# Kernel optimization log

Hardware: AMD Instinct MI355X
Metric: run time of the kernel (lower is better)

The kernel has to match this reference:

```python
import jax, jax.numpy as jnp
import numpy as np

N = 262144          # pixels (512x512 image)
F = 2               # in_features (x, y)
K = 13              # num_frequencies
H = 256             # dim_hidden
OUT = 3             # out_features (RGB)
TILES = [1, 4, 16, 64, 256]   # prod(tile_dims[i]) per layer
PE_DIM = F + 2 * F * K        # 54


def setup_inputs() -> dict:
    key = jax.random.key(0)
    ks = jax.random.split(key, 2 * len(TILES) + 3)
    inp = {"coords": jax.random.uniform(ks[0], (N, F), dtype=jnp.float32)}
    d_in = PE_DIM
    for i, t in enumerate(TILES):
        # kaiming-uniform-like scale; biases init to zero as in the module
        bound = float(np.sqrt(6.0 / d_in))
        inp[f"w{i}"] = jax.random.uniform(ks[1 + i], (t, d_in, H), dtype=jnp.float32,
                                           minval=-bound, maxval=bound)
        inp[f"b{i}"] = jnp.zeros((H,), dtype=jnp.float32)
        d_in = H
    bound = float(np.sqrt(6.0 / H))
    inp["w_last"] = jax.random.uniform(ks[-1], (OUT, H), dtype=jnp.float32,
                                        minval=-bound, maxval=bound)
    inp["b_last"] = jnp.zeros((OUT,), dtype=jnp.float32)
    return inp


def _pos_enc(coords):
    # NeRF positional encoding, concat order: coords, then for each freq i,
    # for each feature j: sin(2^i * pi * c_j), cos(2^i * pi * c_j)
    freqs = (2.0 ** jnp.arange(K, dtype=jnp.float32)) * np.pi      # [K]
    ang = coords[:, None, :] * freqs[None, :, None]                # [N, K, F]
    enc = jnp.stack([jnp.sin(ang), jnp.cos(ang)], axis=-1)         # [N, K, F, 2]
    enc = enc.reshape(coords.shape[0], 2 * K * F)
    return jnp.concatenate([coords, enc], axis=-1)                 # [N, PE_DIM]


def reference(coords, w0, b0, w1, b1, w2, b2, w3, b3, w4, b4, w_last, b_last):
    x = _pos_enc(coords)                                           # [N, 54]
    for w, b in ((w0, b0), (w1, b1), (w2, b2), (w3, b3), (w4, b4)):
        t = w.shape[0]
        x = x.reshape(t, -1, x.shape[-1])                          # [T, N/T, d_in]
        x = jnp.einsum('tnd,tdo->tno', x, w) + b                   # per-tile GEMM
        x = jnp.where(x > 0, x, 0.2 * x)                           # LeakyReLU(0.2)
    x = x.reshape(-1, H)                                           # [N, H]
    return x @ w_last.T + b_last                                   # [N, OUT]
```

## Files before the change

### kernel.cpp

```cpp
#include <hip/hip_runtime.h>
#include <stdint.h>

typedef uint32_t u32;
typedef short s16x8 __attribute__((ext_vector_type(8)));
typedef float f32x16 __attribute__((ext_vector_type(16)));
typedef u32 u32x2 __attribute__((ext_vector_type(2)));
typedef u32 u32x4 __attribute__((ext_vector_type(4)));

#define NPIX   262144
#define HD     256
#define NTHR   512

#define ACT_BYTES  131072
#define WBUF_BYTES 16384
#define LDS_BYTES  (ACT_BYTES + 2 * WBUF_BYTES)

#define B0_OFF  0u
#define B1_OFF  32768u
#define B2_OFF  557056u
#define B3_OFF  2654208u
#define B4_OFF  11042816u
#define BH_OFF  44597248u
#define BLOB_TOTAL 44613632u
#define F_W1 2048u
#define F_W2 34816u
#define F_W3 165888u
#define F_W4 690176u
#define F_WH 2787328u
#define F_END 2788352u

typedef __attribute__((address_space(3))) u32 as3_u32;
typedef __attribute__((address_space(1))) u32 as1_u32;

__device__ __forceinline__ void gload16(const void* g, void* l) {
    __builtin_amdgcn_global_load_lds((const as1_u32*)(uintptr_t)g,
                                     (as3_u32*)(u32)(uintptr_t)l, 16, 0, 0);
}

__device__ __forceinline__ u32 bfpair(float a, float b) {
    u32 ua = __builtin_bit_cast(u32, a);
    u32 ub = __builtin_bit_cast(u32, b);
    ua = (ua + 0x7FFFu + ((ua >> 16) & 1u)) >> 16;
    ub = (ub + 0x7FFFu + ((ub >> 16) & 1u)) >> 16;
    return ua | (ub << 16);
}
__device__ __forceinline__ u32 act_off(int row, int colByte) {
    return (u32)((row << 9) + (colByte ^ ((row & 7) << 4)));
}
__device__ __forceinline__ u32 w_off32(int col, int kByte) {
    return (u32)((col << 6) + (kByte ^ (((col >> 1) & 3) << 4)));
}

extern "C" __global__ __launch_bounds__(256)
void loe_prepass(const float* __restrict__ w0, const float* __restrict__ w1,
                 const float* __restrict__ w2, const float* __restrict__ w3,
                 const float* __restrict__ w4, const float* __restrict__ wl,
                 char* __restrict__ ws)
{
    const u32 f = blockIdx.x * 256 + threadIdx.x;
    if (f >= F_END) return;
    float v[8];
    char* dst;
    if (f < F_W1) {
        const u32 s = f >> 10, r2 = f & 1023, col = r2 >> 2, kg = r2 & 3;
        const u32 k0 = s * 32 + kg * 8;
        #pragma unroll
        for (int j = 0; j < 8; ++j)
            v[j] = (k0 + j < 54) ? w0[(k0 + j) * HD + col] : 0.0f;
        dst = ws + B0_OFF + s * 16384 + w_off32(col, kg * 16);
    } else if (f < F_WH) {
        const float* W; size_t boff; u32 fl;
        if (f < F_W2)      { W = w1; boff = B1_OFF; fl = f - F_W1; }
        else if (f < F_W3) { W = w2; boff = B2_OFF; fl = f - F_W2; }
        else if (f < F_W4) { W = w3; boff = B3_OFF; fl = f - F_W3; }
        else               { W = w4; boff = B4_OFF; fl = f - F_W4; }
        const u32 t = fl >> 13, r = fl & 8191, s = r >> 10, r2 = r & 1023;
        const u32 col = r2 >> 2, kg = r2 & 3;
        const u32 k0 = s * 32 + kg * 8;
        const float* src = W + (size_t)t * 65536 + (size_t)k0 * HD + col;
        #pragma unroll
        for (int j = 0; j < 8; ++j) v[j] = src[(size_t)j * HD];
        dst = ws + boff + (size_t)t * 131072 + s * 16384 + w_off32(col, kg * 16);
    } else {
        const u32 fl = f - F_WH;
        const u32 col = fl >> 5, kg = fl & 31, k0 = kg * 8;
        #pragma unroll
        for (int j = 0; j < 8; ++j)
            v[j] = (col < 3) ? wl[col * HD + k0 + j] : 0.0f;
        dst = ws + BH_OFF + col * 512 + ((kg * 16) ^ ((col & 7) << 4));
    }
    u32x4 pk;
    pk.x = bfpair(v[0], v[1]); pk.y = bfpair(v[2], v[3]);
    pk.z = bfpair(v[4], v[5]); pk.w = bfpair(v[6], v[7]);
    *reinterpret_cast<u32x4*>(dst) = pk;
}

extern "C" __global__ __launch_bounds__(NTHR, 2)
void loe_fused_pre(const float* __restrict__ coords,
                   const float* __restrict__ b0, const float* __restrict__ b1,
                   const float* __restrict__ b2, const float* __restrict__ b3,
                   const float* __restrict__ b4, const float* __restrict__ bl,
                   const char* __restrict__ blob,
                   float* __restrict__ out)
{
    extern __shared__ char lds[];
    char* wbufg = lds + ACT_BYTES;

    const int tid  = threadIdx.x;
    const int lane = tid & 63;
    const int wv   = tid >> 6;
    const int wr   = wv >> 2;
    const int wc   = wv & 3;
    const int l31  = lane & 31;
    const int lhi  = lane >> 5;

    const int bid  = (int)blockIdx.x;
    const int pb   = ((bid & 7) << 7) | (bid >> 3);
    const int pix0 = pb << 8;

    int g = 0;

    auto stage = [&](const char* src, int parity) {
        const char* s0 = src + wv * 2048 + (size_t)lane * 16;
        char* d0 = wbufg + parity * WBUF_BYTES + wv * 2048;
        gload16(s0, d0);
        gload16(s0 + 1024, d0 + 1024);
    };

    const char* b0p = blob + B0_OFF;
    const char* b1p = blob + B1_OFF + (size_t)(pb >> 8) * 131072;
    const char* b2p = blob + B2_OFF + (size_t)(pb >> 6) * 131072;
    const char* b3p = blob + B3_OFF + (size_t)(pb >> 4) * 131072;
    const char* b4p = blob + B4_OFF + (size_t)(pb >> 2) * 131072;
    const char* bHp = blob + BH_OFF;

    stage(b0p, 0);

    {
        const int p = tid >> 1;
        const int h = tid & 1;
        const float2 c2 = reinterpret_cast<const float2*>(coords)[pix0 + p];
        const float cf[2] = {c2.x, c2.y};
        #pragma unroll
        for (int u = 0; u < 32; u += 2) {
            float v[2];
            #pragma unroll
            for (int q = 0; q < 2; ++q) {
                const int c = h * 32 + u + q;
                float val;
                if (c < 2) val = cf[c];
                else if (c - 2 >= 52) val = 0.0f;
                else {
                    const int e = c - 2;
                    const float a = cf[(e >> 1) & 1] * (float)(1 << (e >> 2));
                    val = (e & 1) ? cospif(a) : sinpif(a);
                }
                v[q] = val;
            }
            *reinterpret_cast<u32*>(lds + act_off(p, (h * 32 + u) * 2)) = bfpair(v[0], v[1]);
        }
    }

    f32x16 acc[4][2];

    auto init_acc = [&](const float* Bias) {
        #pragma unroll
        for (int ct = 0; ct < 2; ++ct)
            #pragma unroll
            for (int q = 0; q < 4; ++q) {
                const float4 bv = *reinterpret_cast<const float4*>(Bias + wc * 64 + ct * 32 + q * 8 + lhi * 4);
                #pragma unroll
                for (int pt = 0; pt < 4; ++pt) {
                    acc[pt][ct][q * 4 + 0] = bv.x; acc[pt][ct][q * 4 + 1] = bv.y;
                    acc[pt][ct][q * 4 + 2] = bv.z; acc[pt][ct][q * 4 + 3] = bv.w;
                }
            }
    };

    auto epilogue = [&]() {
        #pragma unroll
        for (int ct = 0; ct < 2; ++ct)
            #pragma unroll
            for (int q = 0; q < 4; ++q) {
                const int oc0 = wc * 64 + ct * 32 + q * 8 + lhi * 4;
                #pragma unroll
                for (int pt = 0; pt < 4; ++pt) {
                    const int p = wr * 128 + pt * 32 + l31;
                    float x[4];
                    #pragma unroll
                    for (int j = 0; j < 4; ++j) {
                        const float v = acc[pt][ct][q * 4 + j];
                        x[j] = fmaxf(v, 0.2f * v);
                    }
                    u32x2 w2v;
                    w2v.x = bfpair(x[0], x[1]);
                    w2v.y = bfpair(x[2], x[3]);
                    *reinterpret_cast<u32x2*>(lds + act_off(p, oc0 * 2)) = w2v;
                }
            }
    };

    auto run_layer = [&](int S, const char* cur, const char* nxt, const float* Bias) {
        init_acc(Bias);
        for (int s = 0; s < S; ++s) {
            __syncthreads();
            const char* pf = (s + 1 < S) ? cur + (size_t)(s + 1) * 16384 : nxt;
            stage(pf, (g + 1) & 1);
            const char* wbw = wbufg + (g & 1) * WBUF_BYTES;
            const int kbase = s * 64;
            #pragma unroll
            for (int kt = 0; kt < 2; ++kt) {
                const int kb = kt * 32 + lhi * 16;
                s16x8 wf[2], af[4];
                #pragma unroll
                for (int ct = 0; ct < 2; ++ct)
                    wf[ct] = *reinterpret_cast<const s16x8*>(wbw + w_off32(wc * 64 + ct * 32 + l31, kb));
                #pragma unroll
                for (int pt = 0; pt < 4; ++pt)
                    af[pt] = *reinterpret_cast<const s16x8*>(lds + act_off(wr * 128 + pt * 32 + l31, kbase + kb));
                #pragma unroll
                for (int pt = 0; pt < 4; ++pt)
                    #pragma unroll
                    for (int ct = 0; ct < 2; ++ct)
                        acc[pt][ct] = __builtin_amdgcn_mfma_f32_32x32x16_bf16(wf[ct], af[pt], acc[pt][ct], 0, 0, 0);
            }
            ++g;
        }
        __syncthreads();
        epilogue();
    };

    run_layer(2, b0p, b1p, b0);
    run_layer(8, b1p, b2p, b1);
    run_layer(8, b2p, b3p, b2);
    run_layer(8, b3p, b4p, b3);
    run_layer(8, b4p, bHp, b4);

    __syncthreads();
    {
        const char* hw = wbufg + (g & 1) * WBUF_BYTES;
        f32x16 a;
        #pragma unroll
        for (int r = 0; r < 16; ++r) a[r] = 0.0f;
        #pragma unroll
        for (int kt = 0; kt < 16; ++kt) {
            const int kb = kt * 32 + lhi * 16;
            s16x8 wf = *reinterpret_cast<const s16x8*>(hw + l31 * 512 + (kb ^ ((l31 & 7) << 4)));
            s16x8 af = *reinterpret_cast<const s16x8*>(lds + act_off(wv * 32 + l31, kb));
            a = __builtin_amdgcn_mfma_f32_32x32x16_bf16(wf, af, a, 0, 0, 0);
        }
        if (lhi == 0) {
            const int p = pix0 + wv * 32 + l31;
            out[p * 3 + 0] = a[0] + bl[0];
            out[p * 3 + 1] = a[1] + bl[1];
            out[p * 3 + 2] = a[2] + bl[2];
        }
    }
}

extern "C" __global__ __launch_bounds__(NTHR, 2)
void loe_fused_fb(const float* __restrict__ coords,
                  const float* __restrict__ w0, const float* __restrict__ b0,
                  const float* __restrict__ w1, const float* __restrict__ b1,
                  const float* __restrict__ w2, const float* __restrict__ b2,
                  const float* __restrict__ w3, const float* __restrict__ b3,
                  const float* __restrict__ w4, const float* __restrict__ b4,
                  const float* __restrict__ wl, const float* __restrict__ bl,
                  float* __restrict__ out)
{
    extern __shared__ char lds[];
    const int tid  = threadIdx.x;
    const int lane = tid & 63;
    const int wv   = tid >> 6;
    const int wr   = wv >> 2;
    const int wc   = wv & 3;
    const int l31  = lane & 31;
    const int lhi  = lane >> 5;
    const int bid  = (int)blockIdx.x;
    const int pb   = ((bid & 7) << 7) | (bid >> 3);
    const int pix0 = pb << 8;
    const int scol = tid & 255;
    const int kh   = tid >> 8;

    float st[16];
    auto load_plain = [&](const float* W, int s) {
        const float* src = W + (size_t)(s * 32 + kh * 16) * HD + scol;
        #pragma unroll
        for (int j = 0; j < 16; ++j) st[j] = src[(size_t)j * HD];
    };
    auto load_guard = [&](const float* W, int s) {
        #pragma unroll
        for (int j = 0; j < 16; ++j) {
            const int k = s * 32 + kh * 16 + j;
            st[j] = (k < 54) ? W[k * HD + scol] : 0.0f;
        }
    };
    load_guard(w0, 0);
    {
        const int p = tid >> 1;
        const int h = tid & 1;
        const float2 c2 = reinterpret_cast<const float2*>(coords)[pix0 + p];
        const float cf[2] = {c2.x, c2.y};
        #pragma unroll
        for (int u = 0; u < 32; u += 2) {
            float v[2];
            #pragma unroll
            for (int q = 0; q < 2; ++q) {
                const int c = h * 32 + u + q;
                float val;
                if (c < 2) val = cf[c];
                else if (c - 2 >= 52) val = 0.0f;
                else {
                    const int e = c - 2;
                    const float a = cf[(e >> 1) & 1] * (float)(1 << (e >> 2));
                    val = (e & 1) ? cospif(a) : sinpif(a);
                }
                v[q] = val;
            }
            *reinterpret_cast<u32*>(lds + act_off(p, (h * 32 + u) * 2)) = bfpair(v[0], v[1]);
        }
    }
    f32x16 acc[4][2];
    int g = 0;
    auto epilogue = [&](const float* Bias) {
        #pragma unroll
        for (int ct = 0; ct < 2; ++ct)
            #pragma unroll
            for (int q = 0; q < 4; ++q) {
                const int oc0 = wc * 64 + ct * 32 + q * 8 + lhi * 4;
                const float4 bv = *reinterpret_cast<const float4*>(Bias + oc0);
                const float bj[4] = {bv.x, bv.y, bv.z, bv.w};
                #pragma unroll
                for (int pt = 0; pt < 4; ++pt) {
                    const int p = wr * 128 + pt * 32 + l31;
                    float x[4];
                    #pragma unroll
                    for (int j = 0; j < 4; ++j) {
                        float v = acc[pt][ct][q * 4 + j] + bj[j];
                        x[j] = (v > 0.0f) ? v : 0.2f * v;
                    }
                    u32x2 wv2;
                    wv2.x = bfpair(x[0], x[1]);
                    wv2.y = bfpair(x[2], x[3]);
                    *reinterpret_cast<u32x2*>(lds + act_off(p, oc0 * 2)) = wv2;
                }
            }
    };
    auto run_layer = [&](int S, const float* Wcur, const float* Wnext,
                         const float* Bias, bool guard) {
        #pragma unroll
        for (int pt = 0; pt < 4; ++pt)
            #pragma unroll
            for (int ct = 0; ct < 2; ++ct)
                #pragma unroll
                for (int r = 0; r < 16; ++r) acc[pt][ct][r] = 0.0f;
        for (int s = 0; s < S; ++s) {
            char* wbw = lds + ACT_BYTES + ((g & 1) ? WBUF_BYTES : 0);
            u32x4 pk0, pk1;
            pk0.x = bfpair(st[0], st[1]);   pk0.y = bfpair(st[2], st[3]);
            pk0.z = bfpair(st[4], st[5]);   pk0.w = bfpair(st[6], st[7]);
            pk1.x = bfpair(st[8], st[9]);   pk1.y = bfpair(st[10], st[11]);
            pk1.z = bfpair(st[12], st[13]); pk1.w = bfpair(st[14], st[15]);
            *reinterpret_cast<u32x4*>(wbw + w_off32(scol, kh * 32))      = pk0;
            *reinterpret_cast<u32x4*>(wbw + w_off32(scol, kh * 32 + 16)) = pk1;
            if (s + 1 < S) { if (guard) load_guard(Wcur, s + 1); else load_plain(Wcur, s + 1); }
            else if (Wnext) load_plain(Wnext, 0);
            __syncthreads();
            const int kbase = s * 64;
            #pragma unroll
            for (int kt = 0; kt < 2; ++kt) {
                const int kb = kt * 32 + lhi * 16;
                s16x8 wf[2], af[4];
                #pragma unroll
                for (int ct = 0; ct < 2; ++ct)
                    wf[ct] = *reinterpret_cast<const s16x8*>(wbw + w_off32(wc * 64 + ct * 32 + l31, kb));
                #pragma unroll
                for (int pt = 0; pt < 4; ++pt)
                    af[pt] = *reinterpret_cast<const s16x8*>(lds + act_off(wr * 128 + pt * 32 + l31, kbase + kb));
                #pragma unroll
                for (int pt = 0; pt < 4; ++pt)
                    #pragma unroll
                    for (int ct = 0; ct < 2; ++ct)
                        acc[pt][ct] = __builtin_amdgcn_mfma_f32_32x32x16_bf16(wf[ct], af[pt], acc[pt][ct], 0, 0, 0);
            }
            ++g;
        }
        __syncthreads();
        epilogue(Bias);
    };
    const float* w1t = w1 + (size_t)(pb >> 8) * 65536;
    const float* w2t = w2 + (size_t)(pb >> 6) * 65536;
    const float* w3t = w3 + (size_t)(pb >> 4) * 65536;
    const float* w4t = w4 + (size_t)(pb >> 2) * 65536;
    run_layer(2, w0,  w1t, b0, true);
    run_layer(8, w1t, w2t, b1, false);
    run_layer(8, w2t, w3t, b2, false);
    run_layer(8, w3t, w4t, b3, false);
    run_layer(8, w4t, nullptr, b4, false);
    char* hw = lds + ACT_BYTES;
    #pragma unroll
    for (int rep = 0; rep < 2; ++rep) {
        const int task = rep * NTHR + tid;
        const int col  = task & 31;
        const int kg   = task >> 5;
        float v[8];
        #pragma unroll
        for (int j = 0; j < 8; ++j)
            v[j] = (col < 3) ? wl[col * HD + kg * 8 + j] : 0.0f;
        u32x4 pk;
        pk.x = bfpair(v[0], v[1]); pk.y = bfpair(v[2], v[3]);
        pk.z = bfpair(v[4], v[5]); pk.w = bfpair(v[6], v[7]);
        *reinterpret_cast<u32x4*>(hw + col * 512 + ((kg * 16) ^ ((col & 7) << 4))) = pk;
    }
    __syncthreads();
    {
        f32x16 a;
        #pragma unroll
        for (int r = 0; r < 16; ++r) a[r] = 0.0f;
        #pragma unroll
        for (int kt = 0; kt < 16; ++kt) {
            const int kb = kt * 32 + lhi * 16;
            s16x8 wf = *reinterpret_cast<const s16x8*>(hw + l31 * 512 + (kb ^ ((l31 & 7) << 4)));
            s16x8 af = *reinterpret_cast<const s16x8*>(lds + act_off(wv * 32 + l31, kb));
            a = __builtin_amdgcn_mfma_f32_32x32x16_bf16(wf, af, a, 0, 0, 0);
        }
        if (lhi == 0) {
            const int p = pix0 + wv * 32 + l31;
            out[p * 3 + 0] = a[0] + bl[0];
            out[p * 3 + 1] = a[1] + bl[1];
            out[p * 3 + 2] = a[2] + bl[2];
        }
    }
}

extern "C" void kernel_launch(void* const* d_in, const int* in_sizes, int n_in,
                              void* d_out, int out_size, void* d_ws, size_t ws_size,
                              hipStream_t stream) {
    (void)in_sizes; (void)n_in; (void)out_size;
    const float* coords = (const float*)d_in[0];
    const float* w0 = (const float*)d_in[1];  const float* b0 = (const float*)d_in[2];
    const float* w1 = (const float*)d_in[3];  const float* b1 = (const float*)d_in[4];
    const float* w2 = (const float*)d_in[5];  const float* b2 = (const float*)d_in[6];
    const float* w3 = (const float*)d_in[7];  const float* b3 = (const float*)d_in[8];
    const float* w4 = (const float*)d_in[9];  const float* b4 = (const float*)d_in[10];
    const float* wl = (const float*)d_in[11]; const float* bl = (const float*)d_in[12];
    float* out = (float*)d_out;

    if (ws_size >= (size_t)BLOB_TOTAL) {
        (void)hipFuncSetAttribute((const void*)loe_fused_pre,
                                  hipFuncAttributeMaxDynamicSharedMemorySize, LDS_BYTES);
        loe_prepass<<<dim3(F_END / 256), dim3(256), 0, stream>>>(
            w0, w1, w2, w3, w4, wl, (char*)d_ws);
        loe_fused_pre<<<dim3(NPIX / 256), dim3(NTHR), LDS_BYTES, stream>>>(
            coords, b0, b1, b2, b3, b4, bl, (const char*)d_ws, out);
    } else {
        (void)hipFuncSetAttribute((const void*)loe_fused_fb,
                                  hipFuncAttributeMaxDynamicSharedMemorySize, LDS_BYTES);
        loe_fused_fb<<<dim3(NPIX / 256), dim3(NTHR), LDS_BYTES, stream>>>(
            coords, w0, b0, w1, b1, w2, b2, w3, b3, w4, b4, wl, bl, out);
    }
}
```

Measured before the change: 188.4 us.

## Load weight MFMA fragments directly from global into registers, drop LDS weight staging

The main kernel now uses 128-pixel blocks of 256 threads, and each wave owns a 64-column slice of every layer. Weight fragments are prepacked in MFMA lane order so they can be read straight from global/L2 into registers, with a one-step software prefetch. This removes the LDS weight double buffer and most per-step barriers and halves LDS to 64KB, which should allow more resident blocks. In exchange each block re-reads full weight tiles from L2 with no LDS sharing across waves, and it processes fewer pixels per block.

```diff
diff --git a/kernel.cpp b/kernel.cpp
--- a/kernel.cpp
+++ b/kernel.cpp
@@ -9,11 +9,11 @@
 
 #define NPIX   262144
 #define HD     256
-#define NTHR   512
-
-#define ACT_BYTES  131072
-#define WBUF_BYTES 16384
-#define LDS_BYTES  (ACT_BYTES + 2 * WBUF_BYTES)
+
+#define FTHR      256
+#define PXB       128
+#define NBLK      (NPIX / PXB)
+#define ACT_LDS   65536
 
 #define B0_OFF  0u
 #define B1_OFF  32768u
@@ -29,13 +29,9 @@
 #define F_WH 2787328u
 #define F_END 2788352u
 
-typedef __attribute__((address_space(3))) u32 as3_u32;
-typedef __attribute__((address_space(1))) u32 as1_u32;
-
-__device__ __forceinline__ void gload16(const void* g, void* l) {
-    __builtin_amdgcn_global_load_lds((const as1_u32*)(uintptr_t)g,
-                                     (as3_u32*)(u32)(uintptr_t)l, 16, 0, 0);
-}
+#define ACT_BYTES  131072
+#define WBUF_BYTES 16384
+#define FB_LDS     (ACT_BYTES + 2 * WBUF_BYTES)
 
 __device__ __forceinline__ u32 bfpair(float a, float b) {
     u32 ua = __builtin_bit_cast(u32, a);
@@ -45,7 +41,7 @@
     return ua | (ub << 16);
 }
 __device__ __forceinline__ u32 act_off(int row, int colByte) {
-    return (u32)((row << 9) + (colByte ^ ((row & 7) << 4)));
+    return (u32)((row << 9) + (colByte ^ ((row & 31) << 4)));
 }
 __device__ __forceinline__ u32 w_off32(int col, int kByte) {
     return (u32)((col << 6) + (kByte ^ (((col >> 1) & 3) << 4)));
@@ -62,32 +58,36 @@
     float v[8];
     char* dst;
     if (f < F_W1) {
-        const u32 s = f >> 10, r2 = f & 1023, col = r2 >> 2, kg = r2 & 3;
-        const u32 k0 = s * 32 + kg * 8;
+        const u32 kk = f >> 9, fb = (f >> 6) & 7, lane = f & 63;
+        const u32 l31 = lane & 31, lhi = lane >> 5;
+        const u32 k0 = kk * 16 + lhi * 8, col = fb * 32 + l31;
         #pragma unroll
         for (int j = 0; j < 8; ++j)
             v[j] = (k0 + j < 54) ? w0[(k0 + j) * HD + col] : 0.0f;
-        dst = ws + B0_OFF + s * 16384 + w_off32(col, kg * 16);
+        dst = ws + B0_OFF + (size_t)f * 16;
     } else if (f < F_WH) {
         const float* W; size_t boff; u32 fl;
         if (f < F_W2)      { W = w1; boff = B1_OFF; fl = f - F_W1; }
         else if (f < F_W3) { W = w2; boff = B2_OFF; fl = f - F_W2; }
         else if (f < F_W4) { W = w3; boff = B3_OFF; fl = f - F_W3; }
         else               { W = w4; boff = B4_OFF; fl = f - F_W4; }
-        const u32 t = fl >> 13, r = fl & 8191, s = r >> 10, r2 = r & 1023;
-        const u32 col = r2 >> 2, kg = r2 & 3;
-        const u32 k0 = s * 32 + kg * 8;
+        const u32 t = fl >> 13, c = fl & 8191;
+        const u32 kk = c >> 9, fb = (c >> 6) & 7, lane = c & 63;
+        const u32 l31 = lane & 31, lhi = lane >> 5;
+        const u32 k0 = kk * 16 + lhi * 8, col = fb * 32 + l31;
         const float* src = W + (size_t)t * 65536 + (size_t)k0 * HD + col;
         #pragma unroll
         for (int j = 0; j < 8; ++j) v[j] = src[(size_t)j * HD];
-        dst = ws + boff + (size_t)t * 131072 + s * 16384 + w_off32(col, kg * 16);
+        dst = ws + boff + (size_t)fl * 16;
     } else {
         const u32 fl = f - F_WH;
-        const u32 col = fl >> 5, kg = fl & 31, k0 = kg * 8;
+        const u32 kk = fl >> 6, lane = fl & 63;
+        const u32 l31 = lane & 31, lhi = lane >> 5;
+        const u32 k0 = kk * 16 + lhi * 8;
         #pragma unroll
         for (int j = 0; j < 8; ++j)
-            v[j] = (col < 3) ? wl[col * HD + k0 + j] : 0.0f;
-        dst = ws + BH_OFF + col * 512 + ((kg * 16) ^ ((col & 7) << 4));
+            v[j] = (l31 < 3) ? wl[l31 * HD + k0 + j] : 0.0f;
+        dst = ws + BH_OFF + (size_t)fl * 16;
     }
     u32x4 pk;
     pk.x = bfpair(v[0], v[1]); pk.y = bfpair(v[2], v[3]);
@@ -95,7 +95,7 @@
     *reinterpret_cast<u32x4*>(dst) = pk;
 }
 
-extern "C" __global__ __launch_bounds__(NTHR, 2)
+extern "C" __global__ __launch_bounds__(FTHR, 2)
 void loe_fused_pre(const float* __restrict__ coords,
                    const float* __restrict__ b0, const float* __restrict__ b1,
                    const float* __restrict__ b2, const float* __restrict__ b3,
@@ -104,37 +104,16 @@
                    float* __restrict__ out)
 {
     extern __shared__ char lds[];
-    char* wbufg = lds + ACT_BYTES;
 
     const int tid  = threadIdx.x;
     const int lane = tid & 63;
     const int wv   = tid >> 6;
-    const int wr   = wv >> 2;
-    const int wc   = wv & 3;
     const int l31  = lane & 31;
     const int lhi  = lane >> 5;
 
     const int bid  = (int)blockIdx.x;
-    const int pb   = ((bid & 7) << 7) | (bid >> 3);
-    const int pix0 = pb << 8;
-
-    int g = 0;
-
-    auto stage = [&](const char* src, int parity) {
-        const char* s0 = src + wv * 2048 + (size_t)lane * 16;
-        char* d0 = wbufg + parity * WBUF_BYTES + wv * 2048;
-        gload16(s0, d0);
-        gload16(s0 + 1024, d0 + 1024);
-    };
-
-    const char* b0p = blob + B0_OFF;
-    const char* b1p = blob + B1_OFF + (size_t)(pb >> 8) * 131072;
-    const char* b2p = blob + B2_OFF + (size_t)(pb >> 6) * 131072;
-    const char* b3p = blob + B3_OFF + (size_t)(pb >> 4) * 131072;
-    const char* b4p = blob + B4_OFF + (size_t)(pb >> 2) * 131072;
-    const char* bHp = blob + BH_OFF;
-
-    stage(b0p, 0);
+    const int pb   = ((bid & 7) << 8) | (bid >> 3);
+    const int pix0 = pb << 7;
 
     {
         const int p = tid >> 1;
@@ -162,13 +141,17 @@
     }
 
     f32x16 acc[4][2];
+    const u32 swz = (u32)(l31 << 4);
+    u32 abase[4];
+    #pragma unroll
+    for (int pt = 0; pt < 4; ++pt) abase[pt] = (u32)((pt * 32 + l31) << 9);
 
     auto init_acc = [&](const float* Bias) {
         #pragma unroll
         for (int ct = 0; ct < 2; ++ct)
             #pragma unroll
             for (int q = 0; q < 4; ++q) {
-                const float4 bv = *reinterpret_cast<const float4*>(Bias + wc * 64 + ct * 32 + q * 8 + lhi * 4);
+                const float4 bv = *reinterpret_cast<const float4*>(Bias + wv * 64 + ct * 32 + q * 8 + lhi * 4);
                 #pragma unroll
                 for (int pt = 0; pt < 4; ++pt) {
                     acc[pt][ct][q * 4 + 0] = bv.x; acc[pt][ct][q * 4 + 1] = bv.y;
@@ -182,72 +165,78 @@
         for (int ct = 0; ct < 2; ++ct)
             #pragma unroll
             for (int q = 0; q < 4; ++q) {
-                const int oc0 = wc * 64 + ct * 32 + q * 8 + lhi * 4;
+                const int oc0 = wv * 64 + ct * 32 + q * 8 + lhi * 4;
                 #pragma unroll
                 for (int pt = 0; pt < 4; ++pt) {
-                    const int p = wr * 128 + pt * 32 + l31;
                     float x[4];
                     #pragma unroll
                     for (int j = 0; j < 4; ++j) {
                         const float v = acc[pt][ct][q * 4 + j];
                         x[j] = fmaxf(v, 0.2f * v);
                     }
-                    u32x2 w2v;
-                    w2v.x = bfpair(x[0], x[1]);
-                    w2v.y = bfpair(x[2], x[3]);
-                    *reinterpret_cast<u32x2*>(lds + act_off(p, oc0 * 2)) = w2v;
+                    u32x2 wo;
+                    wo.x = bfpair(x[0], x[1]);
+                    wo.y = bfpair(x[2], x[3]);
+                    *reinterpret_cast<u32x2*>(lds + act_off(pt * 32 + l31, oc0 * 2)) = wo;
                 }
             }
     };
 
-    auto run_layer = [&](int S, const char* cur, const char* nxt, const float* Bias) {
+    auto run_layer = [&](int KK, const char* wbase, const float* Bias) {
         init_acc(Bias);
-        for (int s = 0; s < S; ++s) {
-            __syncthreads();
-            const char* pf = (s + 1 < S) ? cur + (size_t)(s + 1) * 16384 : nxt;
-            stage(pf, (g + 1) & 1);
-            const char* wbw = wbufg + (g & 1) * WBUF_BYTES;
-            const int kbase = s * 64;
-            #pragma unroll
-            for (int kt = 0; kt < 2; ++kt) {
-                const int kb = kt * 32 + lhi * 16;
-                s16x8 wf[2], af[4];
-                #pragma unroll
-                for (int ct = 0; ct < 2; ++ct)
-                    wf[ct] = *reinterpret_cast<const s16x8*>(wbw + w_off32(wc * 64 + ct * 32 + l31, kb));
-                #pragma unroll
-                for (int pt = 0; pt < 4; ++pt)
-                    af[pt] = *reinterpret_cast<const s16x8*>(lds + act_off(wr * 128 + pt * 32 + l31, kbase + kb));
-                #pragma unroll
-                for (int pt = 0; pt < 4; ++pt)
-                    #pragma unroll
-                    for (int ct = 0; ct < 2; ++ct)
-                        acc[pt][ct] = __builtin_amdgcn_mfma_f32_32x32x16_bf16(wf[ct], af[pt], acc[pt][ct], 0, 0, 0);
-            }
-            ++g;
+        __syncthreads();
+        const char* f0 = wbase + (size_t)(wv * 2) * 1024 + (size_t)lane * 16;
+        u32x4 wA = *reinterpret_cast<const u32x4*>(f0);
+        u32x4 wB = *reinterpret_cast<const u32x4*>(f0 + 1024);
+        #pragma unroll 4
+        for (int kk = 0; kk < KK; ++kk) {
+            const int nk = (kk + 1 < KK) ? kk + 1 : kk;
+            const u32x4 nA = *reinterpret_cast<const u32x4*>(f0 + (size_t)nk * 8192);
+            const u32x4 nB = *reinterpret_cast<const u32x4*>(f0 + (size_t)nk * 8192 + 1024);
+            const u32 cb = (u32)(kk * 32 + lhi * 16) ^ swz;
+            s16x8 af[4];
+            #pragma unroll
+            for (int pt = 0; pt < 4; ++pt)
+                af[pt] = *reinterpret_cast<const s16x8*>(lds + abase[pt] + cb);
+            const s16x8 a = __builtin_bit_cast(s16x8, wA);
+            const s16x8 b = __builtin_bit_cast(s16x8, wB);
+            #pragma unroll
+            for (int pt = 0; pt < 4; ++pt)
+                acc[pt][0] = __builtin_amdgcn_mfma_f32_32x32x16_bf16(a, af[pt], acc[pt][0], 0, 0, 0);
+            #pragma unroll
+            for (int pt = 0; pt < 4; ++pt)
+                acc[pt][1] = __builtin_amdgcn_mfma_f32_32x32x16_bf16(b, af[pt], acc[pt][1], 0, 0, 0);
+            wA = nA; wB = nB;
         }
         __syncthreads();
         epilogue();
     };
 
-    run_layer(2, b0p, b1p, b0);
-    run_layer(8, b1p, b2p, b1);
-    run_layer(8, b2p, b3p, b2);
-    run_layer(8, b3p, b4p, b3);
-    run_layer(8, b4p, bHp, b4);
+    const char* b0p = blob + B0_OFF;
+    const char* b1p = blob + B1_OFF + (size_t)(pb >> 9) * 131072;
+    const char* b2p = blob + B2_OFF + (size_t)(pb >> 7) * 131072;
+    const char* b3p = blob + B3_OFF + (size_t)(pb >> 5) * 131072;
+    const char* b4p = blob + B4_OFF + (size_t)(pb >> 3) * 131072;
+    const char* bHp = blob + BH_OFF;
+
+    run_layer(4,  b0p, b0);
+    run_layer(16, b1p, b1);
+    run_layer(16, b2p, b2);
+    run_layer(16, b3p, b3);
+    run_layer(16, b4p, b4);
 
     __syncthreads();
     {
-        const char* hw = wbufg + (g & 1) * WBUF_BYTES;
         f32x16 a;
         #pragma unroll
         for (int r = 0; r < 16; ++r) a[r] = 0.0f;
-        #pragma unroll
-        for (int kt = 0; kt < 16; ++kt) {
-            const int kb = kt * 32 + lhi * 16;
-            s16x8 wf = *reinterpret_cast<const s16x8*>(hw + l31 * 512 + (kb ^ ((l31 & 7) << 4)));
-            s16x8 af = *reinterpret_cast<const s16x8*>(lds + act_off(wv * 32 + l31, kb));
-            a = __builtin_amdgcn_mfma_f32_32x32x16_bf16(wf, af, a, 0, 0, 0);
+        const u32 hrow = (u32)((wv * 32 + l31) << 9);
+        #pragma unroll 4
+        for (int kk = 0; kk < 16; ++kk) {
+            const u32x4 wh = *reinterpret_cast<const u32x4*>(bHp + (size_t)kk * 1024 + (size_t)lane * 16);
+            const u32 cb = (u32)(kk * 32 + lhi * 16) ^ swz;
+            const s16x8 af = *reinterpret_cast<const s16x8*>(lds + hrow + cb);
+            a = __builtin_amdgcn_mfma_f32_32x32x16_bf16(__builtin_bit_cast(s16x8, wh), af, a, 0, 0, 0);
         }
         if (lhi == 0) {
             const int p = pix0 + wv * 32 + l31;
@@ -258,7 +247,7 @@
     }
 }
 
-extern "C" __global__ __launch_bounds__(NTHR, 2)
+extern "C" __global__ __launch_bounds__(512, 2)
 void loe_fused_fb(const float* __restrict__ coords,
                   const float* __restrict__ w0, const float* __restrict__ b0,
                   const float* __restrict__ w1, const float* __restrict__ b1,
@@ -366,7 +355,6 @@
             if (s + 1 < S) { if (guard) load_guard(Wcur, s + 1); else load_plain(Wcur, s + 1); }
             else if (Wnext) load_plain(Wnext, 0);
             __syncthreads();
-            const int kbase = s * 64;
             #pragma unroll
             for (int kt = 0; kt < 2; ++kt) {
                 const int kb = kt * 32 + lhi * 16;
@@ -376,7 +364,7 @@
                     wf[ct] = *reinterpret_cast<const s16x8*>(wbw + w_off32(wc * 64 + ct * 32 + l31, kb));
                 #pragma unroll
                 for (int pt = 0; pt < 4; ++pt)
-                    af[pt] = *reinterpret_cast<const s16x8*>(lds + act_off(wr * 128 + pt * 32 + l31, kbase + kb));
+                    af[pt] = *reinterpret_cast<const s16x8*>(lds + act_off(wr * 128 + pt * 32 + l31, s * 64 + kb));
                 #pragma unroll
                 for (int pt = 0; pt < 4; ++pt)
                     #pragma unroll
@@ -384,14 +372,16 @@
                         acc[pt][ct] = __builtin_amdgcn_mfma_f32_32x32x16_bf16(wf[ct], af[pt], acc[pt][ct], 0, 0, 0);
             }
             ++g;
-        }
+            __syncthreads();
+        }
+        epilogue(Bias);
         __syncthreads();
-        epilogue(Bias);
     };
     const float* w1t = w1 + (size_t)(pb >> 8) * 65536;
     const float* w2t = w2 + (size_t)(pb >> 6) * 65536;
     const float* w3t = w3 + (size_t)(pb >> 4) * 65536;
     const float* w4t = w4 + (size_t)(pb >> 2) * 65536;
+    __syncthreads();
     run_layer(2, w0,  w1t, b0, true);
     run_layer(8, w1t, w2t, b1, false);
     run_layer(8, w2t, w3t, b2, false);
@@ -400,7 +390,7 @@
     char* hw = lds + ACT_BYTES;
     #pragma unroll
     for (int rep = 0; rep < 2; ++rep) {
-        const int task = rep * NTHR + tid;
+        const int task = rep * 512 + tid;
         const int col  = task & 31;
         const int kg   = task >> 5;
         float v[8];
@@ -448,15 +438,15 @@
 
     if (ws_size >= (size_t)BLOB_TOTAL) {
         (void)hipFuncSetAttribute((const void*)loe_fused_pre,
-                                  hipFuncAttributeMaxDynamicSharedMemorySize, LDS_BYTES);
-        loe_prepass<<<dim3(F_END / 256), dim3(256), 0, stream>>>(
+                                  hipFuncAttributeMaxDynamicSharedMemorySize, ACT_LDS);
+        loe_prepass<<<dim3((F_END + 255) / 256), dim3(256), 0, stream>>>(
             w0, w1, w2, w3, w4, wl, (char*)d_ws);
-        loe_fused_pre<<<dim3(NPIX / 256), dim3(NTHR), LDS_BYTES, stream>>>(
+        loe_fused_pre<<<dim3(NBLK), dim3(FTHR), ACT_LDS, stream>>>(
             coords, b0, b1, b2, b3, b4, bl, (const char*)d_ws, out);
     } else {
         (void)hipFuncSetAttribute((const void*)loe_fused_fb,
-                                  hipFuncAttributeMaxDynamicSharedMemorySize, LDS_BYTES);
-        loe_fused_fb<<<dim3(NPIX / 256), dim3(NTHR), LDS_BYTES, stream>>>(
+                                  hipFuncAttributeMaxDynamicSharedMemorySize, FB_LDS);
+        loe_fused_fb<<<dim3(NPIX / 256), dim3(512), FB_LDS, stream>>>(
             coords, w0, b0, w1, b1, w2, b2, w3, b3, w4, b4, wl, bl, out);
     }
 }
```

Result: no change. 185.8 us (-1.4%).
